# Performance work log

Hardware: AMD Instinct MI355X
Metric: run time of the kernel (lower is better)

## Reference

```python
import jax, jax.numpy as jnp
import numpy as np

TEMP = 0.05
EPS = 1e-6  # both the cosine-sim denom eps and the final log eps


def _cosine(x, y):
    # torch.nn.CosineSimilarity(dim=-1, eps=1e-6):
    # dot(x, y) / max(||x|| * ||y||, eps), broadcasting over leading dims.
    dot = jnp.sum(x * y, axis=-1)
    nx = jnp.linalg.norm(x, axis=-1)
    ny = jnp.linalg.norm(y, axis=-1)
    return dot / jnp.maximum(nx * ny, EPS)


def setup_inputs() -> dict:
    key = jax.random.key(0)
    k1, k2, k3 = jax.random.split(key, 3)
    D, N = 1024, 65536
    return {
        "anchor": jax.random.normal(k1, (D,), dtype=jnp.float32),
        "positive": jax.random.normal(k2, (D,), dtype=jnp.float32),
        "negative": jax.random.normal(k3, (N, D), dtype=jnp.float32),
    }


def reference(anchor, positive, negative):
    # positive similarity: scalar
    pos_sim = _cosine(anchor, positive) / TEMP
    # all negative similarities in one batched pass: [N]
    neg_sim = _cosine(anchor[None, :], negative) / TEMP
    neg_sum = jnp.sum(jnp.exp(neg_sim))  # scalar exp-sum over negatives
    out = -jnp.log(jnp.exp(pos_sim) / neg_sum + EPS)
    return out.reshape(1)  # torch returns shape [1]
```

## Files before the change

kernel.cpp:

```cpp
#include <hip/hip_runtime.h>
#include <math.h>

#define TEMP_INV 20.0f
#define EPS_F 1e-6f

__global__ __launch_bounds__(256) void infonce_neg_pass(
    const float* __restrict__ a,
    const float* __restrict__ neg,
    float* __restrict__ partials,
    int N)
{
    __shared__ float a_lds[1024];
    __shared__ float red[256];

    const int tid = threadIdx.x;

    float4 av = ((const float4*)a)[tid];
    ((float4*)a_lds)[tid] = av;
    red[tid] = av.x * av.x + av.y * av.y + av.z * av.z + av.w * av.w;
    __syncthreads();
    for (int s = 128; s > 0; s >>= 1) {
        if (tid < s) red[tid] += red[tid + s];
        __syncthreads();
    }
    const float anorm = sqrtf(red[0]);
    __syncthreads();

    const int lane = tid & 63;
    const int wave = tid >> 6;

    float4 areg[4];
    #pragma unroll
    for (int j = 0; j < 4; ++j)
        areg[j] = ((const float4*)a_lds)[j * 64 + lane];

    const int gwave = blockIdx.x * 4 + wave;
    const int total_waves = gridDim.x * 4;
    const int chunk = (N + total_waves - 1) / total_waves;
    const int base = gwave * chunk;
    const int end = (base + chunk < N) ? base + chunk : N;

    float local = 0.0f;
    for (int row = base; row < end; row += 2) {
        const bool two = (row + 1 < end);
        const float4* r0 = (const float4*)neg + (size_t)row * 256;
        const float4* r1 = r0 + 256;

        float4 v0[4], v1[4];
        #pragma unroll
        for (int j = 0; j < 4; ++j) v0[j] = r0[j * 64 + lane];
        if (two) {
            #pragma unroll
            for (int j = 0; j < 4; ++j) v1[j] = r1[j * 64 + lane];
        }

        float d0 = 0.f, n0 = 0.f, d1 = 0.f, n1 = 0.f;
        #pragma unroll
        for (int j = 0; j < 4; ++j) {
            d0 += v0[j].x * areg[j].x + v0[j].y * areg[j].y
                + v0[j].z * areg[j].z + v0[j].w * areg[j].w;
            n0 += v0[j].x * v0[j].x + v0[j].y * v0[j].y
                + v0[j].z * v0[j].z + v0[j].w * v0[j].w;
        }
        if (two) {
            #pragma unroll
            for (int j = 0; j < 4; ++j) {
                d1 += v1[j].x * areg[j].x + v1[j].y * areg[j].y
                    + v1[j].z * areg[j].z + v1[j].w * areg[j].w;
                n1 += v1[j].x * v1[j].x + v1[j].y * v1[j].y
                    + v1[j].z * v1[j].z + v1[j].w * v1[j].w;
            }
        }

        #pragma unroll
        for (int off = 32; off > 0; off >>= 1) {
            d0 += __shfl_xor(d0, off);
            n0 += __shfl_xor(n0, off);
            d1 += __shfl_xor(d1, off);
            n1 += __shfl_xor(n1, off);
        }

        const float s0 = d0 / fmaxf(anorm * sqrtf(n0), EPS_F) * TEMP_INV;
        local += expf(s0);
        if (two) {
            const float s1 = d1 / fmaxf(anorm * sqrtf(n1), EPS_F) * TEMP_INV;
            local += expf(s1);
        }
    }

    if (lane == 0) red[wave] = local;
    __syncthreads();
    if (tid == 0)
        partials[blockIdx.x] = red[0] + red[1] + red[2] + red[3];
}

__global__ __launch_bounds__(256) void infonce_finalize(
    const float* __restrict__ a,
    const float* __restrict__ p,
    const float* __restrict__ partials,
    int nparts,
    float* __restrict__ out)
{
    __shared__ float r0[256], r1[256], r2[256], r3[256];
    const int tid = threadIdx.x;

    float4 av = ((const float4*)a)[tid];
    float4 pv = ((const float4*)p)[tid];
    r0[tid] = av.x * pv.x + av.y * pv.y + av.z * pv.z + av.w * pv.w;
    r1[tid] = av.x * av.x + av.y * av.y + av.z * av.z + av.w * av.w;
    r2[tid] = pv.x * pv.x + pv.y * pv.y + pv.z * pv.z + pv.w * pv.w;

    float nloc = 0.0f;
    for (int i = tid; i < nparts; i += 256) nloc += partials[i];
    r3[tid] = nloc;
    __syncthreads();

    for (int s = 128; s > 0; s >>= 1) {
        if (tid < s) {
            r0[tid] += r0[tid + s];
            r1[tid] += r1[tid + s];
            r2[tid] += r2[tid + s];
            r3[tid] += r3[tid + s];
        }
        __syncthreads();
    }

    if (tid == 0) {
        const float pos_sim =
            r0[0] / fmaxf(sqrtf(r1[0]) * sqrtf(r2[0]), EPS_F) * TEMP_INV;
        out[0] = -logf(expf(pos_sim) / r3[0] + EPS_F);
    }
}

extern "C" void kernel_launch(void* const* d_in, const int* in_sizes, int n_in,
                              void* d_out, int out_size, void* d_ws, size_t ws_size,
                              hipStream_t stream) {
    const float* a   = (const float*)d_in[0];
    const float* p   = (const float*)d_in[1];
    const float* neg = (const float*)d_in[2];
    const int D = in_sizes[0];
    const int N = in_sizes[2] / D;
    float* out      = (float*)d_out;
    float* partials = (float*)d_ws;

    int nblocks = 2048;
    if (nblocks * 4 > N) nblocks = (N + 3) / 4;

    infonce_neg_pass<<<nblocks, 256, 0, stream>>>(a, neg, partials, N);
    infonce_finalize<<<1, 256, 0, stream>>>(a, p, partials, nblocks, out);
}
```

Baseline: 48.96 us.

## Software-pipeline negative row loads and compute anchor norm per wave

Register double-buffers the next pair of negative rows so their global loads are in flight while the current pair is reduced and exponentiated. It also drops the LDS staging and block-wide tree reduction of the anchor, having each wave load the anchor directly and compute its norm with wave shuffles. This removes several barriers from the kernel prologue, at the cost of more registers per thread, which may lower occupancy.

```diff
diff --git a/kernel.cpp b/kernel.cpp
--- a/kernel.cpp
+++ b/kernel.cpp
@@ -10,29 +10,26 @@
     float* __restrict__ partials,
     int N)
 {
-    __shared__ float a_lds[1024];
-    __shared__ float red[256];
+    __shared__ float red[4];
 
     const int tid = threadIdx.x;
-
-    float4 av = ((const float4*)a)[tid];
-    ((float4*)a_lds)[tid] = av;
-    red[tid] = av.x * av.x + av.y * av.y + av.z * av.z + av.w * av.w;
-    __syncthreads();
-    for (int s = 128; s > 0; s >>= 1) {
-        if (tid < s) red[tid] += red[tid + s];
-        __syncthreads();
-    }
-    const float anorm = sqrtf(red[0]);
-    __syncthreads();
-
     const int lane = tid & 63;
     const int wave = tid >> 6;
 
     float4 areg[4];
     #pragma unroll
     for (int j = 0; j < 4; ++j)
-        areg[j] = ((const float4*)a_lds)[j * 64 + lane];
+        areg[j] = ((const float4*)a)[j * 64 + lane];
+
+    float an = 0.0f;
+    #pragma unroll
+    for (int j = 0; j < 4; ++j)
+        an += areg[j].x * areg[j].x + areg[j].y * areg[j].y
+            + areg[j].z * areg[j].z + areg[j].w * areg[j].w;
+    #pragma unroll
+    for (int off = 32; off > 0; off >>= 1)
+        an += __shfl_xor(an, off);
+    const float anorm = sqrtf(an);
 
     const int gwave = blockIdx.x * 4 + wave;
     const int total_waves = gridDim.x * 4;
@@ -41,34 +38,53 @@
     const int end = (base + chunk < N) ? base + chunk : N;
 
     float local = 0.0f;
-    for (int row = base; row < end; row += 2) {
-        const bool two = (row + 1 < end);
-        const float4* r0 = (const float4*)neg + (size_t)row * 256;
-        const float4* r1 = r0 + 256;
 
-        float4 v0[4], v1[4];
-        #pragma unroll
-        for (int j = 0; j < 4; ++j) v0[j] = r0[j * 64 + lane];
+    float4 c0[4], c1[4], n0x[4], n1x[4];
+    {
+        const bool have = base < end;
+        const bool two = base + 1 < end;
+        const float4* r0 = (const float4*)neg + (size_t)base * 256;
+        if (have) {
+            #pragma unroll
+            for (int j = 0; j < 4; ++j) c0[j] = r0[j * 64 + lane];
+        }
         if (two) {
             #pragma unroll
-            for (int j = 0; j < 4; ++j) v1[j] = r1[j * 64 + lane];
+            for (int j = 0; j < 4; ++j) c1[j] = r0[256 + j * 64 + lane];
+        }
+    }
+
+    for (int row = base; row < end; row += 2) {
+        const bool ctwo = (row + 1 < end);
+        const int nrow = row + 2;
+        const bool nhave = nrow < end;
+        const bool ntwo = nrow + 1 < end;
+
+        const float4* rn = (const float4*)neg + (size_t)nrow * 256;
+        if (nhave) {
+            #pragma unroll
+            for (int j = 0; j < 4; ++j) n0x[j] = rn[j * 64 + lane];
+        }
+        if (ntwo) {
+            #pragma unroll
+            for (int j = 0; j < 4; ++j) n1x[j] = rn[256 + j * 64 + lane];
         }
 
         float d0 = 0.f, n0 = 0.f, d1 = 0.f, n1 = 0.f;
         #pragma unroll
         for (int j = 0; j < 4; ++j) {
-            d0 += v0[j].x * areg[j].x + v0[j].y * areg[j].y
-                + v0[j].z * areg[j].z + v0[j].w * areg[j].w;
-            n0 += v0[j].x * v0[j].x + v0[j].y * v0[j].y
-                + v0[j].z * v0[j].z + v0[j].w * v0[j].w;
+            d0 += c0[j].x * areg[j].x + c0[j].y * areg[j].y
+                + c0[j].z * areg[j].z + c0[j].w * areg[j].w;
+            n0 += c0[j].x * c0[j].x + c0[j].y * c0[j].y
+                + c0[j].z * c0[j].z + c0[j].w * c0[j].w;
         }
-        if (two) {
+        if (ctwo) {
             #pragma unroll
             for (int j = 0; j < 4; ++j) {
-                d1 += v1[j].x * areg[j].x + v1[j].y * areg[j].y
-                    + v1[j].z * areg[j].z + v1[j].w * areg[j].w;
-                n1 += v1[j].x * v1[j].x + v1[j].y * v1[j].y
-                    + v1[j].z * v1[j].z + v1[j].w * v1[j].w;
+                d1 += c1[j].x * areg[j].x + c1[j].y * areg[j].y
+                    + c1[j].z * areg[j].z + c1[j].w * areg[j].w;
+                n1 += c1[j].x * c1[j].x + c1[j].y * c1[j].y
+                    + c1[j].z * c1[j].z + c1[j].w * c1[j].w;
             }
         }
 
@@ -82,10 +98,13 @@
 
         const float s0 = d0 / fmaxf(anorm * sqrtf(n0), EPS_F) * TEMP_INV;
         local += expf(s0);
-        if (two) {
+        if (ctwo) {
             const float s1 = d1 / fmaxf(anorm * sqrtf(n1), EPS_F) * TEMP_INV;
             local += expf(s1);
         }
+
+        #pragma unroll
+        for (int j = 0; j < 4; ++j) { c0[j] = n0x[j]; c1[j] = n1x[j]; }
     }
 
     if (lane == 0) red[wave] = local;
```

Result: no change. 48.50 us (-0.9%).
